# Optimization experiments

Hardware: AMD Instinct MI355X
Metric: run time of the kernel (lower is better)

The kernel has to match this reference:

```python
import jax, jax.numpy as jnp
import numpy as np
import math

B, N, CS, CZ = 2, 512, 384, 128
H, C, PQ, PV = 12, 16, 4, 8
EPS = 1e-8

def _quat_to_rot(q):
    q = q / jnp.linalg.norm(q, axis=-1, keepdims=True)
    a, b, c, d = q[..., 0], q[..., 1], q[..., 2], q[..., 3]
    return jnp.stack([
        jnp.stack([a*a+b*b-c*c-d*d, 2*(b*c-a*d), 2*(b*d+a*c)], -1),
        jnp.stack([2*(b*c+a*d), a*a-b*b+c*c-d*d, 2*(c*d-a*b)], -1),
        jnp.stack([2*(b*d-a*c), 2*(c*d+a*b), a*a-b*b-c*c+d*d], -1)], -2)

def setup_inputs() -> dict:
    key = jax.random.key(0)
    ks = jax.random.split(key, 12)
    def lin(k, out_f, in_f):
        return jax.random.normal(k, (out_f, in_f), jnp.float32) * math.sqrt(1.0 / in_f)
    inp = {}
    inp['single'] = jax.random.normal(ks[0], (B, N, CS), jnp.float32)
    inp['pair'] = jax.random.normal(ks[1], (B, N, N, CZ), jnp.float32)
    inp['rotations'] = _quat_to_rot(jax.random.normal(ks[2], (B, N, 4), jnp.float32))
    inp['translations'] = jax.random.normal(ks[3], (B, N, 3), jnp.float32) * 10.0
    inp['wq'] = lin(ks[4], H*C, CS); inp['bq'] = jnp.zeros((H*C,), jnp.float32)
    inp['wkv'] = lin(ks[5], 2*H*C, CS); inp['bkv'] = jnp.zeros((2*H*C,), jnp.float32)
    inp['wqp'] = lin(ks[6], 3*H*PQ, CS); inp['bqp'] = jnp.zeros((3*H*PQ,), jnp.float32)
    inp['wkvp'] = lin(ks[7], 3*H*(PQ+PV), CS); inp['bkvp'] = jnp.zeros((3*H*(PQ+PV),), jnp.float32)
    inp['wb'] = lin(ks[8], H, CZ); inp['bb'] = jnp.zeros((H,), jnp.float32)
    out_in = H*C + H*PV*4 + H*CZ  # scalar + (x,y,z,norm) points + pair
    inp['wo'] = lin(ks[9], CS, out_in); inp['bo'] = jnp.zeros((CS,), jnp.float32)
    inp['head_weights'] = jax.random.normal(ks[10], (H,), jnp.float32) * 0.1
    return inp

def _ipa(single, pair, rotations, translations, wq, bq, wkv, bkv, wqp, bqp, wkvp, bkvp, wb, bb, wo, bo, head_weights):
    b_, n_ = single.shape[0], single.shape[1]
    # scalar q/k/v
    q = (single @ wq.T + bq).reshape(b_, n_, H, C)
    kv = (single @ wkv.T + bkv).reshape(b_, n_, H, 2*C)
    k, v = kv[..., :C], kv[..., C:]
    # point q/k/v in local frames (chunk into x,y,z then stack, per _project_points)
    def proj_pts(w, bvec, P):
        raw = single @ w.T + bvec
        xc, yc, zc = jnp.split(raw, 3, axis=-1)
        return jnp.stack([xc, yc, zc], -1).reshape(b_, n_, H, P, 3)
    q_pts = proj_pts(wqp, bqp, PQ)
    kv_pts = proj_pts(wkvp, bkvp, PQ + PV)
    k_pts, v_pts = kv_pts[..., :PQ, :], kv_pts[..., PQ:, :]
    # apply rigid frames: global = R @ p + t
    def to_global(p):
        return jnp.einsum('biop,bihqp->bihqo', rotations, p) + translations[:, :, None, None, :]
    qg, kg, vg = to_global(q_pts), to_global(k_pts), to_global(v_pts)
    # scalar logits + pair bias
    bias = pair @ wb.T + bb  # [B,N,N,H]
    logits = jnp.einsum('bihc,bjhc->bhij', q, k) * math.sqrt(1.0 / (3.0 * C))
    logits = logits + math.sqrt(1.0 / 3.0) * bias.transpose(0, 3, 1, 2)
    # point-distance logits
    d2 = jnp.sum((qg[:, :, None] - kg[:, None]) ** 2, axis=-1)  # [B,N,N,H,PQ]
    gamma = jax.nn.softplus(head_weights)  # [H]
    wpt = math.sqrt(1.0 / (3.0 * PQ * 4.5))
    pt_logits = -0.5 * wpt * jnp.sum(d2, axis=-1) * gamma  # [B,N,N,H]
    attn = jax.nn.softmax(logits + pt_logits.transpose(0, 3, 1, 2), axis=-1)  # [B,H,N,N]
    # assemble output features
    out_scalar = jnp.einsum('bhij,bjhc->bihc', attn, v).reshape(b_, n_, H*C)
    rp_g = jnp.einsum('bhij,bjhpc->bihpc', attn, vg)
    # back to local frame: R^T @ (p - t)
    rp_l = jnp.einsum('bipo,bihqp->bihqo', rotations, rp_g - translations[:, :, None, None, :])
    norms = jnp.sqrt(jnp.sum(rp_l ** 2, -1) + EPS).reshape(b_, n_, H*PV)
    rp_l = rp_l.reshape(b_, n_, H*PV, 3)
    out_pair = jnp.einsum('bhij,bijd->bihd', attn, pair).reshape(b_, n_, H*CZ)
    feats = jnp.concatenate([out_scalar, rp_l[..., 0], rp_l[..., 1], rp_l[..., 2], norms, out_pair], -1)
    return feats @ wo.T + bo

def reference(single, pair, rotations, translations, wq, bq, wkv, bkv, wqp, bqp, wkvp, bkvp, wb, bb, wo, bo, head_weights):
    return _ipa(single, pair, rotations, translations, wq, bq, wkv, bkv, wqp, bqp, wkvp, bkvp, wb, bb, wo, bo, head_weights)
```

## Files before the change

### kernel.cpp

```cpp
#include <hip/hip_runtime.h>
#include <hip/hip_bf16.h>
#include <math.h>

#define NB 2
#define NN 512
#define CSD 384
#define CZD 128
#define NH 12
#define NC 16
#define NPQ 4
#define NPV 8
#define HC 192
#define QPDIM 144
#define FEATD 2112
#define VALLD 512
#define WPT 0.13608276348795434f
#define RS3C 0.14433756729740643f
#define RS3 0.5773502691896258f

typedef __attribute__((ext_vector_type(8))) short short8;
typedef __attribute__((ext_vector_type(4))) float f32x4;

static __device__ inline unsigned short f2bf(float x) {
    __hip_bfloat16 h = __float2bfloat16(x);
    return *reinterpret_cast<unsigned short*>(&h);
}
static __device__ inline unsigned short bflo(float x) {
    __hip_bfloat16 h = __float2bfloat16(x);
    return f2bf(x - __bfloat162float(h));
}

#define R_S0 393216
#define R_S1 (R_S0 + 73728)
#define R_S2 (R_S1 + 147456)
#define R_S3 (R_S2 + 55296)
#define R_S4 (R_S3 + 165888)
#define R_S5 (R_S4 + 811008)
#define R_S6 (R_S5 + 2048)
__global__ __launch_bounds__(256) void k_cvt(
    const float* __restrict__ single, const float* __restrict__ wq,
    const float* __restrict__ wkv, const float* __restrict__ wqp,
    const float* __restrict__ wkvp, const float* __restrict__ wo,
    const float* __restrict__ wb,
    unsigned short* __restrict__ singleb, unsigned short* __restrict__ wallb,
    unsigned short* __restrict__ wob, unsigned short* __restrict__ wbb)
{
    int gid = blockIdx.x * 256 + threadIdx.x;
    int e = gid * 4;
    if (e >= R_S6) return;
    if (e >= R_S5) {
        int c = e - R_S5;
        int hh = c >> 7;
        ushort4 o;
        if (hh < 12) {
            float4 v = *(const float4*)(wb + hh * 128 + (c & 127));
            o.x = f2bf(v.x); o.y = f2bf(v.y); o.z = f2bf(v.z); o.w = f2bf(v.w);
        } else { o.x = 0; o.y = 0; o.z = 0; o.w = 0; }
        *(ushort4*)(wbb + c) = o;
        return;
    }
    const float* src; unsigned short* dst;
    if (e < R_S0)      { src = single + e;          dst = singleb + e; }
    else if (e < R_S1) { src = wq + (e - R_S0);     dst = wallb + (e - R_S0); }
    else if (e < R_S2) { src = wkv + (e - R_S1);    dst = wallb + 73728 + (e - R_S1); }
    else if (e < R_S3) { src = wqp + (e - R_S2);    dst = wallb + 221184 + (e - R_S2); }
    else if (e < R_S4) { src = wkvp + (e - R_S3);   dst = wallb + 276480 + (e - R_S3); }
    else               { src = wo + (e - R_S4);     dst = wob + (e - R_S4); }
    float4 v = *(const float4*)src;
    ushort4 o;
    o.x = f2bf(v.x); o.y = f2bf(v.y); o.z = f2bf(v.z); o.w = f2bf(v.w);
    *(ushort4*)dst = o;
}

__global__ __launch_bounds__(256) void k_gemm1(
    const unsigned short* __restrict__ A, const unsigned short* __restrict__ Bm,
    float* __restrict__ Cr)
{
    int w = threadIdx.x >> 6, lane = threadIdx.x & 63;
    int rt = blockIdx.x;
    int ct = blockIdx.y * 4 + w;
    int r = lane & 15, kq = lane >> 4;
    const unsigned short* ap = A  + (size_t)(rt * 16 + r) * 384 + kq * 8;
    const unsigned short* bp = Bm + (size_t)(ct * 16 + r) * 384 + kq * 8;
    f32x4 acc = {0.f, 0.f, 0.f, 0.f};
    #pragma unroll 4
    for (int ks = 0; ks < 12; ++ks) {
        short8 av = *(const short8*)(ap + ks * 32);
        short8 bv = *(const short8*)(bp + ks * 32);
        acc = __builtin_amdgcn_mfma_f32_16x16x32_bf16(av, bv, acc, 0, 0, 0);
    }
    int crow = rt * 16 + kq * 4;
    int ccol = ct * 16 + r;
    #pragma unroll
    for (int i = 0; i < 4; ++i)
        Cr[(size_t)(crow + i) * 1152 + ccol] = acc[i];
}

__global__ __launch_bounds__(256) void k_post(
    const float* __restrict__ praw, const float* __restrict__ rot, const float* __restrict__ trans,
    const float* __restrict__ hw,
    const float* __restrict__ bq, const float* __restrict__ bkv,
    const float* __restrict__ bqp, const float* __restrict__ bkvp,
    float* __restrict__ vall,
    unsigned short* __restrict__ qhat, unsigned short* __restrict__ khat,
    float* __restrict__ qn2, float* __restrict__ kn2)
{
    __shared__ float s_q[192], s_k[192], s_qp[QPDIM], s_kvp[432];
    __shared__ float s_qg[144], s_kg[144];
    __shared__ float s_sh[12];
    const int t = threadIdx.x;
    const int row = blockIdx.x;
    const int b = row >> 9;
    const int i = row & 511;

    if (t < 12) {
        float sp = log1pf(expf(hw[t]));
        s_sh[t] = RS3C / (WPT * sp);
    }
    const float* pr = praw + (size_t)row * 1152;
    for (int idx = t; idx < 1152; idx += 256) {
        float v = pr[idx];
        if (idx < 192) {
            s_q[idx] = v + bq[idx];
        } else if (idx < 576) {
            int f = idx - 192; float x = v + bkv[f];
            int h = f >> 5, cc = f & 31;
            if (cc < 16) s_k[h * 16 + cc] = x;
            else         vall[(size_t)row * VALLD + h * 16 + cc - 16] = x;
        } else if (idx < 720) {
            int f = idx - 576; s_qp[f] = v + bqp[f];
        } else {
            int f = idx - 720; s_kvp[f] = v + bkvp[f];
        }
    }
    __syncthreads();

    if (t < 192) {
        const float* R = rot + (size_t)row * 9;
        const float* T = trans + (size_t)row * 3;
        float lx, ly, lz; float* dst;
        if (t < 48) {
            lx = s_qp[t]; ly = s_qp[48 + t]; lz = s_qp[96 + t];
            dst = s_qg + t * 3;
        } else if (t < 96) {
            int idx = t - 48; int fb = (idx >> 2) * 12 + (idx & 3);
            lx = s_kvp[fb]; ly = s_kvp[144 + fb]; lz = s_kvp[288 + fb];
            dst = s_kg + idx * 3;
        } else {
            int idx = t - 96; int fb = (idx >> 3) * 12 + 4 + (idx & 7);
            lx = s_kvp[fb]; ly = s_kvp[144 + fb]; lz = s_kvp[288 + fb];
            dst = vall + (size_t)row * VALLD + 192 + idx * 3;
        }
        dst[0] = R[0] * lx + R[1] * ly + R[2] * lz + T[0];
        dst[1] = R[3] * lx + R[4] * ly + R[5] * lz + T[1];
        dst[2] = R[6] * lx + R[7] * ly + R[8] * lz + T[2];
    }
    __syncthreads();

    if (t < 24) {
        int h = t % 12;
        const float* g = (t < 12) ? (s_qg + h * 12) : (s_kg + h * 12);
        float s = 0.f;
        #pragma unroll
        for (int e = 0; e < 12; ++e) s += g[e] * g[e];
        float* dst = (t < 12) ? qn2 : kn2;
        dst[((size_t)b * 12 + h) * 512 + i] = s;
    }

    for (int idx = t; idx < 768; idx += 256) {
        int side = idx >= 384;
        int li = side ? (idx - 384) : idx;
        int h = li >> 5, s2 = li & 31;
        unsigned short o[2];
        #pragma unroll
        for (int u = 0; u < 2; ++u) {
            int k = 2 * s2 + u;
            unsigned short val = 0;
            if (!side) {
                if (k < 16)      val = f2bf(s_sh[h] * s_q[h * 16 + k]);
                else if (k < 28) val = f2bf(s_qg[h * 12 + k - 16]);
                else if (k < 40) val = f2bf(s_qg[h * 12 + k - 28]);
                else if (k < 52) val = bflo(s_qg[h * 12 + k - 40]);
            } else {
                if (k < 16)      val = f2bf(s_k[h * 16 + k]);
                else if (k < 28) val = f2bf(s_kg[h * 12 + k - 16]);
                else if (k < 40) val = bflo(s_kg[h * 12 + k - 28]);
                else if (k < 52) val = f2bf(s_kg[h * 12 + k - 40]);
            }
            o[u] = val;
        }
        unsigned short* dst = (side ? khat : qhat) + (((size_t)b * 12 + h) * 512 + i) * 64 + 2 * s2;
        *(ushort2*)dst = make_ushort2(o[0], o[1]);
    }
}

__global__ __launch_bounds__(256) void k_qk(
    const unsigned short* __restrict__ qhat, const unsigned short* __restrict__ khat,
    const float* __restrict__ qn2, const float* __restrict__ kn2,
    const float* __restrict__ hw, float* __restrict__ plog)
{
    int w = threadIdx.x >> 6, lane = threadIdx.x & 63;
    int bh = blockIdx.x;
    int i0 = (blockIdx.y >> 3) * 64;
    int j0 = (blockIdx.y & 7) * 64;
    int r = lane & 15, kq = lane >> 4;
    float sp = log1pf(expf(hw[bh % 12]));
    float m = WPT * sp;
    float coef = -0.5f * m;

    const unsigned short* ap = qhat + ((size_t)bh * 512 + i0 + w * 16 + r) * 64 + kq * 8;
    short8 a0 = *(const short8*)(ap);
    short8 a1 = *(const short8*)(ap + 32);
    const unsigned short* bpb = khat + ((size_t)bh * 512 + j0 + r) * 64 + kq * 8;
    f32x4 acc[4];
    #pragma unroll
    for (int jt = 0; jt < 4; ++jt) {
        short8 b0 = *(const short8*)(bpb + (size_t)jt * 1024);
        short8 b1 = *(const short8*)(bpb + (size_t)jt * 1024 + 32);
        f32x4 a = {0.f, 0.f, 0.f, 0.f};
        a = __builtin_amdgcn_mfma_f32_16x16x32_bf16(a0, b0, a, 0, 0, 0);
        a = __builtin_amdgcn_mfma_f32_16x16x32_bf16(a1, b1, a, 0, 0, 0);
        acc[jt] = a;
    }
    int crow = i0 + w * 16 + kq * 4;
    const float* qn = qn2 + (size_t)bh * 512;
    const float* kn = kn2 + (size_t)bh * 512;
    #pragma unroll
    for (int jt = 0; jt < 4; ++jt) {
        int ccol = j0 + jt * 16 + r;
        float knv = kn[ccol];
        #pragma unroll
        for (int ii = 0; ii < 4; ++ii)
            plog[((size_t)bh * 512 + crow + ii) * 512 + ccol] =
                m * acc[jt][ii] + coef * (qn[crow + ii] + knv);
    }
}

__global__ __launch_bounds__(512) void k_av(
    const float* __restrict__ pair, const float* __restrict__ rot, const float* __restrict__ trans,
    const unsigned short* __restrict__ wbb, const float* __restrict__ bb,
    const float* __restrict__ plog, const float* __restrict__ vall,
    unsigned short* __restrict__ featsb)
{
    __shared__ float attn12[12][521];
    __shared__ float rp2_s[288];
    __shared__ float redv[3][480];
    __shared__ float rot_s[9], trans_s[3];

    const int t = threadIdx.x;
    const int row_i = blockIdx.x;
    const int b = row_i >> 9;
    const size_t bbase = (size_t)b * NN;
    const int w = t >> 6, lane = t & 63;
    const int r = lane & 15, kq = lane >> 4;

    if (t < 9) rot_s[t] = rot[(size_t)row_i * 9 + t];
    if (t >= 9 && t < 12) trans_s[t - 9] = trans[(size_t)row_i * 3 + (t - 9)];

    {
        const unsigned short* bp = wbb + r * 128 + kq * 8;
        short8 bfrag[4];
        #pragma unroll
        for (int ks = 0; ks < 4; ++ks) bfrag[ks] = *(const short8*)(bp + ks * 32);
        float bbv = (r < 12) ? bb[r] : 0.f;
        #pragma unroll
        for (int tt = 0; tt < 4; ++tt) {
            int tile = w + tt * 8;
            const float* ap = pair + ((size_t)row_i * NN + tile * 16 + r) * CZD + kq * 8;
            float4 p[8];
            #pragma unroll
            for (int ks = 0; ks < 4; ++ks) {
                p[2 * ks]     = *(const float4*)(ap + ks * 32);
                p[2 * ks + 1] = *(const float4*)(ap + ks * 32 + 4);
            }
            f32x4 acc = {0.f, 0.f, 0.f, 0.f};
            #pragma unroll
            for (int ks = 0; ks < 4; ++ks) {
                short8 av;
                av[0] = (short)f2bf(p[2*ks].x);   av[1] = (short)f2bf(p[2*ks].y);
                av[2] = (short)f2bf(p[2*ks].z);   av[3] = (short)f2bf(p[2*ks].w);
                av[4] = (short)f2bf(p[2*ks+1].x); av[5] = (short)f2bf(p[2*ks+1].y);
                av[6] = (short)f2bf(p[2*ks+1].z); av[7] = (short)f2bf(p[2*ks+1].w);
                acc = __builtin_amdgcn_mfma_f32_16x16x32_bf16(av, bfrag[ks], acc, 0, 0, 0);
            }
            if (r < 12) {
                #pragma unroll
                for (int ii = 0; ii < 4; ++ii)
                    attn12[r][tile * 16 + kq * 4 + ii] = RS3 * (acc[ii] + bbv);
            }
        }
    }
    __syncthreads();

    #pragma unroll
    for (int it = 0; it < 3; ++it) {
        int idx4 = it * 512 + t;
        int h = idx4 >> 7;
        int j4 = (idx4 & 127) * 4;
        const float* lp = plog + (((size_t)b * 12 + h) * 512 + (row_i & 511)) * 512 + j4;
        float4 lv = *(const float4*)lp;
        attn12[h][j4 + 0] += lv.x;
        attn12[h][j4 + 1] += lv.y;
        attn12[h][j4 + 2] += lv.z;
        attn12[h][j4 + 3] += lv.w;
    }
    __syncthreads();

    for (int hh = w; hh < 12; hh += 8) {
        float vreg[8];
        float mx = -1e30f;
        #pragma unroll
        for (int s = 0; s < 8; ++s) { vreg[s] = attn12[hh][lane + 64 * s]; mx = fmaxf(mx, vreg[s]); }
        #pragma unroll
        for (int off = 32; off >= 1; off >>= 1) mx = fmaxf(mx, __shfl_xor(mx, off, 64));
        float ssum = 0.f;
        #pragma unroll
        for (int s = 0; s < 8; ++s) { vreg[s] = __expf(vreg[s] - mx); ssum += vreg[s]; }
        #pragma unroll
        for (int off = 32; off >= 1; off >>= 1) ssum += __shfl_xor(ssum, off, 64);
        float inv = 1.0f / ssum;
        #pragma unroll
        for (int s = 0; s < 8; ++s) attn12[hh][lane + 64 * s] = vreg[s] * inv;
    }
    __syncthreads();

    unsigned short* frow = featsb + (size_t)row_i * FEATD;

    {
        const int jp = lane >> 2;
        const int dg = lane & 3;
        const int d0 = w * 16 + dg * 4;
        float4 acc12[12];
        #pragma unroll
        for (int hh = 0; hh < 12; ++hh) acc12[hh] = make_float4(0.f, 0.f, 0.f, 0.f);
        const float* pb = pair + (size_t)row_i * NN * CZD + d0;
        for (int jj = 0; jj < 32; ++jj) {
            int j = jj * 16 + jp;
            float4 p4 = *(const float4*)(pb + (size_t)j * CZD);
            #pragma unroll
            for (int hh = 0; hh < 12; ++hh) {
                float a = attn12[hh][j];
                acc12[hh].x += a * p4.x; acc12[hh].y += a * p4.y;
                acc12[hh].z += a * p4.z; acc12[hh].w += a * p4.w;
            }
        }
        #pragma unroll
        for (int off = 4; off <= 32; off <<= 1) {
            #pragma unroll
            for (int hh = 0; hh < 12; ++hh) {
                acc12[hh].x += __shfl_xor(acc12[hh].x, off, 64);
                acc12[hh].y += __shfl_xor(acc12[hh].y, off, 64);
                acc12[hh].z += __shfl_xor(acc12[hh].z, off, 64);
                acc12[hh].w += __shfl_xor(acc12[hh].w, off, 64);
            }
        }
        if (jp == 0) {
            #pragma unroll
            for (int hh = 0; hh < 12; ++hh) {
                ushort4 ov;
                ov.x = f2bf(acc12[hh].x); ov.y = f2bf(acc12[hh].y);
                ov.z = f2bf(acc12[hh].z); ov.w = f2bf(acc12[hh].w);
                *(ushort4*)(frow + 576 + hh * CZD + d0) = ov;
            }
        }
    }

    {
        const int g4 = t & 127;
        const int jp = t >> 7;
        const bool active = (g4 < 120);
        const int c = 4 * g4;
        int arow = 0;
        if (active) arow = (c < 192) ? (c >> 4) : ((c - 192) / 24);
        float ax = 0.f, ay = 0.f, az = 0.f, aw = 0.f;
        if (active) {
            const float* vb = vall + bbase * VALLD + c;
            const float* ar = attn12[arow];
            for (int jj = 0; jj < 128; ++jj) {
                int j = 4 * jj + jp;
                float a = ar[j];
                float4 v4 = *(const float4*)(vb + (size_t)j * VALLD);
                ax += a * v4.x; ay += a * v4.y; az += a * v4.z; aw += a * v4.w;
            }
        }
        if (jp > 0 && active) {
            float4 st = {ax, ay, az, aw};
            *(float4*)&redv[jp - 1][c] = st;
        }
        __syncthreads();
        if (jp == 0 && active) {
            float4 r1 = *(const float4*)&redv[0][c];
            float4 r2 = *(const float4*)&redv[1][c];
            float4 r3 = *(const float4*)&redv[2][c];
            float o0 = ax + r1.x + r2.x + r3.x;
            float o1 = ay + r1.y + r2.y + r3.y;
            float o2 = az + r1.z + r2.z + r3.z;
            float o3 = aw + r1.w + r2.w + r3.w;
            if (c < 192) {
                ushort4 ov; ov.x = f2bf(o0); ov.y = f2bf(o1); ov.z = f2bf(o2); ov.w = f2bf(o3);
                *(ushort4*)(frow + c) = ov;
            } else {
                rp2_s[c - 192] = o0; rp2_s[c - 191] = o1;
                rp2_s[c - 190] = o2; rp2_s[c - 189] = o3;
            }
        }
    }
    __syncthreads();

    if (t < 96) {
        int h = t >> 3, p = t & 7;
        float d0 = rp2_s[h * 24 + p * 3 + 0] - trans_s[0];
        float d1 = rp2_s[h * 24 + p * 3 + 1] - trans_s[1];
        float d2v = rp2_s[h * 24 + p * 3 + 2] - trans_s[2];
        float l0 = rot_s[0] * d0 + rot_s[3] * d1 + rot_s[6] * d2v;
        float l1 = rot_s[1] * d0 + rot_s[4] * d1 + rot_s[7] * d2v;
        float l2 = rot_s[2] * d0 + rot_s[5] * d1 + rot_s[8] * d2v;
        float nrm = sqrtf(l0 * l0 + l1 * l1 + l2 * l2 + 1e-8f);
        int hp = h * 8 + p;
        frow[192 + hp] = f2bf(l0);
        frow[288 + hp] = f2bf(l1);
        frow[384 + hp] = f2bf(l2);
        frow[480 + hp] = f2bf(nrm);
    }
}

__global__ __launch_bounds__(256) void k_gemm2(
    const unsigned short* __restrict__ A, const unsigned short* __restrict__ Bm,
    const float* __restrict__ bo, float* __restrict__ out)
{
    int w = threadIdx.x >> 6, lane = threadIdx.x & 63;
    int rt = blockIdx.x;
    int ct = blockIdx.y * 4 + w;
    int r = lane & 15, kq = lane >> 4;
    const unsigned short* ap = A  + (size_t)(rt * 16 + r) * FEATD + kq * 8;
    const unsigned short* bp = Bm + (size_t)(ct * 16 + r) * FEATD + kq * 8;
    f32x4 acc = {0.f, 0.f, 0.f, 0.f};
    #pragma unroll 2
    for (int ks = 0; ks < 66; ++ks) {
        short8 av = *(const short8*)(ap + ks * 32);
        short8 bv = *(const short8*)(bp + ks * 32);
        acc = __builtin_amdgcn_mfma_f32_16x16x32_bf16(av, bv, acc, 0, 0, 0);
    }
    int crow = rt * 16 + kq * 4;
    int ccol = ct * 16 + r;
    float bv = bo[ccol];
    #pragma unroll
    for (int i = 0; i < 4; ++i)
        out[(size_t)(crow + i) * CSD + ccol] = acc[i] + bv;
}

extern "C" void kernel_launch(void* const* d_in, const int* in_sizes, int n_in,
                              void* d_out, int out_size, void* d_ws, size_t ws_size,
                              hipStream_t stream) {
    const float* single = (const float*)d_in[0];
    const float* pair   = (const float*)d_in[1];
    const float* rot    = (const float*)d_in[2];
    const float* trans  = (const float*)d_in[3];
    const float* wq     = (const float*)d_in[4];
    const float* bq     = (const float*)d_in[5];
    const float* wkv    = (const float*)d_in[6];
    const float* bkv    = (const float*)d_in[7];
    const float* wqp    = (const float*)d_in[8];
    const float* bqp    = (const float*)d_in[9];
    const float* wkvp   = (const float*)d_in[10];
    const float* bkvp   = (const float*)d_in[11];
    const float* wb     = (const float*)d_in[12];
    const float* bb     = (const float*)d_in[13];
    const float* wo     = (const float*)d_in[14];
    const float* bo     = (const float*)d_in[15];
    const float* hw     = (const float*)d_in[16];
    float* out = (float*)d_out;

    float* ws = (float*)d_ws;
    float* plog    = ws;
    float* projraw = ws;
    float* vall    = ws + 6291456;
    unsigned short* qhat = (unsigned short*)(vall + 524288);
    unsigned short* khat = (unsigned short*)((float*)qhat + 393216);
    float* qn2     = (float*)khat + 393216;
    float* kn2     = qn2 + 12288;
    unsigned short* featsb  = (unsigned short*)(kn2 + 12288);
    unsigned short* singleb = (unsigned short*)((float*)featsb + 1081344);
    unsigned short* wallb   = (unsigned short*)((float*)singleb + 196608);
    unsigned short* wob     = (unsigned short*)((float*)wallb + 221184);
    unsigned short* wbb     = wob + 811008;

    hipLaunchKernelGGL(k_cvt, dim3(1610), dim3(256), 0, stream,
                       single, wq, wkv, wqp, wkvp, wo, wb, singleb, wallb, wob, wbb);
    hipLaunchKernelGGL(k_gemm1, dim3(64, 18), dim3(256), 0, stream, singleb, wallb, projraw);
    hipLaunchKernelGGL(k_post, dim3(1024), dim3(256), 0, stream,
                       projraw, rot, trans, hw, bq, bkv, bqp, bkvp,
                       vall, qhat, khat, qn2, kn2);
    hipLaunchKernelGGL(k_qk, dim3(24, 64), dim3(256), 0, stream,
                       qhat, khat, qn2, kn2, hw, plog);
    hipLaunchKernelGGL(k_av, dim3(1024), dim3(512), 0, stream,
                       pair, rot, trans, wbb, bb, plog, vall, featsb);
    hipLaunchKernelGGL(k_gemm2, dim3(64, 6), dim3(256), 0, stream, featsb, wob, bo, out);
}
```

Measured before the change: 191.9 us.

## Move attention-weighted value and pair reductions onto bf16 MFMA with split kernels

The scalar FMA loops in k_av that reduced attention against pair features and against values/points are replaced. The pair reduction now runs on a 16x16x32 bf16 MFMA with strided pair loads, and k_av writes a bf16 copy of the attention matrix to global memory. A new k_avg kernel computes attn·V on MFMA using a transposed bf16 value layout built in k_post, with points split into hi/lo bf16 parts. A small k_rp kernel applies the inverse frame transform. This adds two launches, an extra attention round trip through global memory and bf16 precision on the pair path, in exchange for moving the heavy FP32 FMA work onto matrix units.

```diff
diff --git a/kernel.cpp b/kernel.cpp
--- a/kernel.cpp
+++ b/kernel.cpp
@@ -13,7 +13,6 @@
 #define HC 192
 #define QPDIM 144
 #define FEATD 2112
-#define VALLD 512
 #define WPT 0.13608276348795434f
 #define RS3C 0.14433756729740643f
 #define RS3 0.5773502691896258f
@@ -101,12 +100,12 @@
     const float* __restrict__ hw,
     const float* __restrict__ bq, const float* __restrict__ bkv,
     const float* __restrict__ bqp, const float* __restrict__ bkvp,
-    float* __restrict__ vall,
+    unsigned short* __restrict__ vallT2,
     unsigned short* __restrict__ qhat, unsigned short* __restrict__ khat,
     float* __restrict__ qn2, float* __restrict__ kn2)
 {
-    __shared__ float s_q[192], s_k[192], s_qp[QPDIM], s_kvp[432];
-    __shared__ float s_qg[144], s_kg[144];
+    __shared__ float s_q[192], s_k[192], s_v[192], s_qp[QPDIM], s_kvp[432];
+    __shared__ float s_qg[144], s_kg[144], s_vg[288];
     __shared__ float s_sh[12];
     const int t = threadIdx.x;
     const int row = blockIdx.x;
@@ -126,7 +125,7 @@
             int f = idx - 192; float x = v + bkv[f];
             int h = f >> 5, cc = f & 31;
             if (cc < 16) s_k[h * 16 + cc] = x;
-            else         vall[(size_t)row * VALLD + h * 16 + cc - 16] = x;
+            else         s_v[h * 16 + cc - 16] = x;
         } else if (idx < 720) {
             int f = idx - 576; s_qp[f] = v + bqp[f];
         } else {
@@ -149,7 +148,7 @@
         } else {
             int idx = t - 96; int fb = (idx >> 3) * 12 + 4 + (idx & 7);
             lx = s_kvp[fb]; ly = s_kvp[144 + fb]; lz = s_kvp[288 + fb];
-            dst = vall + (size_t)row * VALLD + 192 + idx * 3;
+            dst = s_vg + idx * 3;
         }
         dst[0] = R[0] * lx + R[1] * ly + R[2] * lz + T[0];
         dst[1] = R[3] * lx + R[4] * ly + R[5] * lz + T[1];
@@ -165,6 +164,15 @@
         for (int e = 0; e < 12; ++e) s += g[e] * g[e];
         float* dst = (t < 12) ? qn2 : kn2;
         dst[((size_t)b * 12 + h) * 512 + i] = s;
+    }
+
+    for (int c = t; c < 768; c += 256) {
+        int h = c >> 6, cp = c & 63;
+        unsigned short v;
+        if (cp < 16)      v = f2bf(s_v[h * 16 + cp]);
+        else if (cp < 40) v = f2bf(s_vg[h * 24 + cp - 16]);
+        else              v = bflo(s_vg[h * 24 + cp - 40]);
+        vallT2[((size_t)(b * 12 + h) * 64 + cp) * 512 + i] = v;
     }
 
     for (int idx = t; idx < 768; idx += 256) {
@@ -237,25 +245,19 @@
 }
 
 __global__ __launch_bounds__(512) void k_av(
-    const float* __restrict__ pair, const float* __restrict__ rot, const float* __restrict__ trans,
+    const float* __restrict__ pair,
     const unsigned short* __restrict__ wbb, const float* __restrict__ bb,
-    const float* __restrict__ plog, const float* __restrict__ vall,
-    unsigned short* __restrict__ featsb)
+    const float* __restrict__ plog,
+    unsigned short* __restrict__ attnb, unsigned short* __restrict__ featsb)
 {
     __shared__ float attn12[12][521];
-    __shared__ float rp2_s[288];
-    __shared__ float redv[3][480];
-    __shared__ float rot_s[9], trans_s[3];
 
     const int t = threadIdx.x;
     const int row_i = blockIdx.x;
     const int b = row_i >> 9;
-    const size_t bbase = (size_t)b * NN;
+    const int i_loc = row_i & 511;
     const int w = t >> 6, lane = t & 63;
     const int r = lane & 15, kq = lane >> 4;
-
-    if (t < 9) rot_s[t] = rot[(size_t)row_i * 9 + t];
-    if (t >= 9 && t < 12) trans_s[t - 9] = trans[(size_t)row_i * 3 + (t - 9)];
 
     {
         const unsigned short* bp = wbb + r * 128 + kq * 8;
@@ -297,7 +299,7 @@
         int idx4 = it * 512 + t;
         int h = idx4 >> 7;
         int j4 = (idx4 & 127) * 4;
-        const float* lp = plog + (((size_t)b * 12 + h) * 512 + (row_i & 511)) * 512 + j4;
+        const float* lp = plog + (((size_t)b * 12 + h) * 512 + i_loc) * 512 + j4;
         float4 lv = *(const float4*)lp;
         attn12[h][j4 + 0] += lv.x;
         attn12[h][j4 + 1] += lv.y;
@@ -324,98 +326,106 @@
     }
     __syncthreads();
 
-    unsigned short* frow = featsb + (size_t)row_i * FEATD;
+    for (int idx = t; idx < 768; idx += 512) {
+        int h = idx >> 6, jc = idx & 63;
+        ushort4 o0, o1;
+        o0.x = f2bf(attn12[h][jc * 8 + 0]); o0.y = f2bf(attn12[h][jc * 8 + 1]);
+        o0.z = f2bf(attn12[h][jc * 8 + 2]); o0.w = f2bf(attn12[h][jc * 8 + 3]);
+        o1.x = f2bf(attn12[h][jc * 8 + 4]); o1.y = f2bf(attn12[h][jc * 8 + 5]);
+        o1.z = f2bf(attn12[h][jc * 8 + 6]); o1.w = f2bf(attn12[h][jc * 8 + 7]);
+        unsigned short* gp = attnb + (((size_t)(b * 12 + h) * 512 + i_loc)) * 512 + jc * 8;
+        *(ushort4*)gp = o0;
+        *(ushort4*)(gp + 4) = o1;
+    }
+    __syncthreads();
 
     {
-        const int jp = lane >> 2;
-        const int dg = lane & 3;
-        const int d0 = w * 16 + dg * 4;
-        float4 acc12[12];
-        #pragma unroll
-        for (int hh = 0; hh < 12; ++hh) acc12[hh] = make_float4(0.f, 0.f, 0.f, 0.f);
-        const float* pb = pair + (size_t)row_i * NN * CZD + d0;
-        for (int jj = 0; jj < 32; ++jj) {
-            int j = jj * 16 + jp;
-            float4 p4 = *(const float4*)(pb + (size_t)j * CZD);
+        const int d0 = w * 16;
+        const int hr = (r < 12) ? r : 11;
+        const unsigned short* arow = attnb + (((size_t)(b * 12 + hr) * 512 + i_loc)) * 512 + kq * 8;
+        const float* pbase = pair + (size_t)row_i * NN * CZD + d0 + r;
+        f32x4 acc = {0.f, 0.f, 0.f, 0.f};
+        for (int ks = 0; ks < 16; ++ks) {
+            int jb = ks * 32 + kq * 8;
+            float x0 = pbase[(size_t)(jb + 0) * CZD];
+            float x1 = pbase[(size_t)(jb + 1) * CZD];
+            float x2 = pbase[(size_t)(jb + 2) * CZD];
+            float x3 = pbase[(size_t)(jb + 3) * CZD];
+            float x4 = pbase[(size_t)(jb + 4) * CZD];
+            float x5 = pbase[(size_t)(jb + 5) * CZD];
+            float x6 = pbase[(size_t)(jb + 6) * CZD];
+            float x7 = pbase[(size_t)(jb + 7) * CZD];
+            short8 av = *(const short8*)(arow + ks * 32);
+            short8 bv;
+            bv[0] = (short)f2bf(x0); bv[1] = (short)f2bf(x1);
+            bv[2] = (short)f2bf(x2); bv[3] = (short)f2bf(x3);
+            bv[4] = (short)f2bf(x4); bv[5] = (short)f2bf(x5);
+            bv[6] = (short)f2bf(x6); bv[7] = (short)f2bf(x7);
+            acc = __builtin_amdgcn_mfma_f32_16x16x32_bf16(av, bv, acc, 0, 0, 0);
+        }
+        unsigned short* frow = featsb + (size_t)row_i * FEATD;
+        if (kq < 3) {
             #pragma unroll
-            for (int hh = 0; hh < 12; ++hh) {
-                float a = attn12[hh][j];
-                acc12[hh].x += a * p4.x; acc12[hh].y += a * p4.y;
-                acc12[hh].z += a * p4.z; acc12[hh].w += a * p4.w;
-            }
-        }
-        #pragma unroll
-        for (int off = 4; off <= 32; off <<= 1) {
-            #pragma unroll
-            for (int hh = 0; hh < 12; ++hh) {
-                acc12[hh].x += __shfl_xor(acc12[hh].x, off, 64);
-                acc12[hh].y += __shfl_xor(acc12[hh].y, off, 64);
-                acc12[hh].z += __shfl_xor(acc12[hh].z, off, 64);
-                acc12[hh].w += __shfl_xor(acc12[hh].w, off, 64);
-            }
-        }
-        if (jp == 0) {
-            #pragma unroll
-            for (int hh = 0; hh < 12; ++hh) {
-                ushort4 ov;
-                ov.x = f2bf(acc12[hh].x); ov.y = f2bf(acc12[hh].y);
-                ov.z = f2bf(acc12[hh].z); ov.w = f2bf(acc12[hh].w);
-                *(ushort4*)(frow + 576 + hh * CZD + d0) = ov;
-            }
-        }
-    }
-
-    {
-        const int g4 = t & 127;
-        const int jp = t >> 7;
-        const bool active = (g4 < 120);
-        const int c = 4 * g4;
-        int arow = 0;
-        if (active) arow = (c < 192) ? (c >> 4) : ((c - 192) / 24);
-        float ax = 0.f, ay = 0.f, az = 0.f, aw = 0.f;
-        if (active) {
-            const float* vb = vall + bbase * VALLD + c;
-            const float* ar = attn12[arow];
-            for (int jj = 0; jj < 128; ++jj) {
-                int j = 4 * jj + jp;
-                float a = ar[j];
-                float4 v4 = *(const float4*)(vb + (size_t)j * VALLD);
-                ax += a * v4.x; ay += a * v4.y; az += a * v4.z; aw += a * v4.w;
-            }
-        }
-        if (jp > 0 && active) {
-            float4 st = {ax, ay, az, aw};
-            *(float4*)&redv[jp - 1][c] = st;
-        }
-        __syncthreads();
-        if (jp == 0 && active) {
-            float4 r1 = *(const float4*)&redv[0][c];
-            float4 r2 = *(const float4*)&redv[1][c];
-            float4 r3 = *(const float4*)&redv[2][c];
-            float o0 = ax + r1.x + r2.x + r3.x;
-            float o1 = ay + r1.y + r2.y + r3.y;
-            float o2 = az + r1.z + r2.z + r3.z;
-            float o3 = aw + r1.w + r2.w + r3.w;
-            if (c < 192) {
-                ushort4 ov; ov.x = f2bf(o0); ov.y = f2bf(o1); ov.z = f2bf(o2); ov.w = f2bf(o3);
-                *(ushort4*)(frow + c) = ov;
-            } else {
-                rp2_s[c - 192] = o0; rp2_s[c - 191] = o1;
-                rp2_s[c - 190] = o2; rp2_s[c - 189] = o3;
-            }
-        }
-    }
-    __syncthreads();
-
+            for (int ii = 0; ii < 4; ++ii)
+                frow[576 + (kq * 4 + ii) * CZD + d0 + r] = f2bf(acc[ii]);
+        }
+    }
+}
+
+__global__ __launch_bounds__(512) void k_avg(
+    const unsigned short* __restrict__ attnb, const unsigned short* __restrict__ vallT2,
+    float* __restrict__ rpg, unsigned short* __restrict__ featsb)
+{
+    int bh = blockIdx.x;
+    int itile = blockIdx.y;
+    int b = bh / 12, h = bh % 12;
+    int w = threadIdx.x >> 6, lane = threadIdx.x & 63;
+    int mt = w >> 2, nt = w & 3;
+    int r = lane & 15, kq = lane >> 4;
+    int i0 = itile * 32 + mt * 16;
+    const unsigned short* ap = attnb + ((size_t)bh * 512 + i0 + r) * 512 + kq * 8;
+    const unsigned short* bp = vallT2 + ((size_t)bh * 64 + nt * 16 + r) * 512 + kq * 8;
+    f32x4 acc = {0.f, 0.f, 0.f, 0.f};
+    #pragma unroll
+    for (int ks = 0; ks < 16; ++ks) {
+        short8 av = *(const short8*)(ap + ks * 32);
+        short8 bv = *(const short8*)(bp + ks * 32);
+        acc = __builtin_amdgcn_mfma_f32_16x16x32_bf16(av, bv, acc, 0, 0, 0);
+    }
+    int cp = nt * 16 + r;
+    #pragma unroll
+    for (int ii = 0; ii < 4; ++ii) {
+        int i = i0 + kq * 4 + ii;
+        size_t rowg = (size_t)b * 512 + i;
+        if (nt == 0) {
+            featsb[rowg * FEATD + h * 16 + r] = f2bf(acc[ii]);
+        } else {
+            rpg[rowg * 576 + h * 48 + (cp - 16)] = acc[ii];
+        }
+    }
+}
+
+__global__ __launch_bounds__(128) void k_rp(
+    const float* __restrict__ rpg, const float* __restrict__ rot, const float* __restrict__ trans,
+    unsigned short* __restrict__ featsb)
+{
+    __shared__ float rot_s[9], trans_s[3];
+    int row = blockIdx.x, t = threadIdx.x;
+    if (t < 9) rot_s[t] = rot[(size_t)row * 9 + t];
+    if (t >= 9 && t < 12) trans_s[t - 9] = trans[(size_t)row * 3 + (t - 9)];
+    __syncthreads();
     if (t < 96) {
         int h = t >> 3, p = t & 7;
-        float d0 = rp2_s[h * 24 + p * 3 + 0] - trans_s[0];
-        float d1 = rp2_s[h * 24 + p * 3 + 1] - trans_s[1];
-        float d2v = rp2_s[h * 24 + p * 3 + 2] - trans_s[2];
+        const float* rp = rpg + (size_t)row * 576 + h * 48;
+        float g0 = rp[p * 3 + 0] + rp[24 + p * 3 + 0];
+        float g1 = rp[p * 3 + 1] + rp[24 + p * 3 + 1];
+        float g2 = rp[p * 3 + 2] + rp[24 + p * 3 + 2];
+        float d0 = g0 - trans_s[0], d1 = g1 - trans_s[1], d2v = g2 - trans_s[2];
         float l0 = rot_s[0] * d0 + rot_s[3] * d1 + rot_s[6] * d2v;
         float l1 = rot_s[1] * d0 + rot_s[4] * d1 + rot_s[7] * d2v;
         float l2 = rot_s[2] * d0 + rot_s[5] * d1 + rot_s[8] * d2v;
         float nrm = sqrtf(l0 * l0 + l1 * l1 + l2 * l2 + 1e-8f);
+        unsigned short* frow = featsb + (size_t)row * FEATD;
         int hp = h * 8 + p;
         frow[192 + hp] = f2bf(l0);
         frow[288 + hp] = f2bf(l1);
@@ -474,26 +484,31 @@
     float* ws = (float*)d_ws;
     float* plog    = ws;
     float* projraw = ws;
-    float* vall    = ws + 6291456;
-    unsigned short* qhat = (unsigned short*)(vall + 524288);
-    unsigned short* khat = (unsigned short*)((float*)qhat + 393216);
-    float* qn2     = (float*)khat + 393216;
-    float* kn2     = qn2 + 12288;
-    unsigned short* featsb  = (unsigned short*)(kn2 + 12288);
-    unsigned short* singleb = (unsigned short*)((float*)featsb + 1081344);
-    unsigned short* wallb   = (unsigned short*)((float*)singleb + 196608);
-    unsigned short* wob     = (unsigned short*)((float*)wallb + 221184);
-    unsigned short* wbb     = wob + 811008;
+    unsigned short* qhat = (unsigned short*)(ws + 6291456);
+    unsigned short* khat = (unsigned short*)(ws + 6684672);
+    float* qn2     = ws + 7077888;
+    float* kn2     = ws + 7090176;
+    unsigned short* featsb  = (unsigned short*)(ws + 7102464);
+    unsigned short* singleb = (unsigned short*)(ws + 8183808);
+    unsigned short* wallb   = (unsigned short*)(ws + 8380416);
+    unsigned short* wob     = (unsigned short*)(ws + 8601600);
+    unsigned short* wbb     = (unsigned short*)(ws + 9007104);
+    unsigned short* vallT2  = (unsigned short*)(ws + 9008128);
+    unsigned short* attnb   = (unsigned short*)(ws + 9401344);
+    float* rpg     = ws + 12547072;
 
     hipLaunchKernelGGL(k_cvt, dim3(1610), dim3(256), 0, stream,
                        single, wq, wkv, wqp, wkvp, wo, wb, singleb, wallb, wob, wbb);
     hipLaunchKernelGGL(k_gemm1, dim3(64, 18), dim3(256), 0, stream, singleb, wallb, projraw);
     hipLaunchKernelGGL(k_post, dim3(1024), dim3(256), 0, stream,
                        projraw, rot, trans, hw, bq, bkv, bqp, bkvp,
-                       vall, qhat, khat, qn2, kn2);
+                       vallT2, qhat, khat, qn2, kn2);
     hipLaunchKernelGGL(k_qk, dim3(24, 64), dim3(256), 0, stream,
                        qhat, khat, qn2, kn2, hw, plog);
     hipLaunchKernelGGL(k_av, dim3(1024), dim3(512), 0, stream,
-                       pair, rot, trans, wbb, bb, plog, vall, featsb);
+                       pair, wbb, bb, plog, attnb, featsb);
+    hipLaunchKernelGGL(k_avg, dim3(24, 16), dim3(512), 0, stream,
+                       attnb, vallT2, rpg, featsb);
+    hipLaunchKernelGGL(k_rp, dim3(1024), dim3(128), 0, stream, rpg, rot, trans, featsb);
     hipLaunchKernelGGL(k_gemm2, dim3(64, 6), dim3(256), 0, stream, featsb, wob, bo, out);
 }
```

New measurement: 187.6 us. 1.02x faster.
